# Kernel optimization log

Hardware: AMD Instinct MI355X
Metric: run time of the kernel (lower is better)

Reference implementation:

```python
import jax, jax.numpy as jnp
import numpy as np

N_QUBITS = 16
N_LAYERS = 8
BATCH = 512


def _apply_1q(st, U, wire):
    """Apply a 2x2 (or batched [B,2,2]) unitary on `wire` of st [B]+[2]*n."""
    st2 = jnp.moveaxis(st, wire + 1, -1)
    if U.ndim == 3:  # batched (input-encoding) gate
        out = jnp.einsum('sab,s...b->s...a', U, st2)
    else:
        out = jnp.einsum('ab,...b->...a', U, st2)
    return jnp.moveaxis(out, -1, wire + 1)


def _apply_cnot(st, c, t):
    """CNOT(control=c, target=t) on st [B]+[2]*n; axis of wire w is w+1."""
    s0, s1 = jnp.split(st, 2, axis=c + 1)
    s1 = jnp.flip(s1, axis=t + 1)  # X on target within control=1 block
    return jnp.concatenate([s0, s1], axis=c + 1)


def _rot_mats(w):
    """PennyLane Rot(phi,theta,omega)=RZ(omega)RY(theta)RZ(phi); w:[n,3] -> [n,2,2]."""
    phi, theta, omega = w[:, 0], w[:, 1], w[:, 2]
    c = jnp.cos(theta / 2).astype(jnp.complex64)
    s = jnp.sin(theta / 2).astype(jnp.complex64)
    ep = jnp.exp(-0.5j * (phi + omega))  # complex64
    em = jnp.exp(-0.5j * (phi - omega))
    m00 = ep * c
    m01 = -jnp.conj(em) * s
    m10 = em * s
    m11 = jnp.conj(ep) * c
    return jnp.stack([jnp.stack([m00, m01], -1), jnp.stack([m10, m11], -1)], -2)


def _circuit(x, weights):
    B, n = x.shape
    # |0...0> state, shape [B] + [2]*n
    st = jnp.zeros((B,) + (2,) * n, jnp.complex64)
    st = st.at[(slice(None),) + (0,) * n].set(1.0)
    # RY(pi * x_i) encoding on each wire (batched gates)
    a = (jnp.pi * x) / 2
    ca, sa = jnp.cos(a), jnp.sin(a)
    for i in range(n):
        U = jnp.stack([jnp.stack([ca[:, i], -sa[:, i]], -1),
                       jnp.stack([sa[:, i], ca[:, i]], -1)], -2).astype(jnp.complex64)
        st = _apply_1q(st, U, i)
    # StronglyEntanglingLayers: per-layer Rot on each wire, then ring of CNOTs
    for l in range(N_LAYERS):
        mats = _rot_mats(weights[l])
        for i in range(n):
            st = _apply_1q(st, mats[i], i)
        r = (l % (n - 1)) + 1  # default PennyLane range pattern
        for i in range(n):
            st = _apply_cnot(st, i, (i + r) % n)
    # <Z_i> = P(bit_i = 0) - P(bit_i = 1)
    p = st.real ** 2 + st.imag ** 2
    outs = []
    for i in range(n):
        marg = jnp.sum(p, axis=tuple(ax for ax in range(1, n + 1) if ax != i + 1))  # [B,2]
        outs.append(marg[:, 0] - marg[:, 1])
    return jnp.stack(outs, axis=-1).astype(jnp.float32)  # [B, n]


def setup_inputs() -> dict:
    key = jax.random.key(0)
    k1, k2 = jax.random.split(key)
    x = jax.random.uniform(k1, (BATCH, N_QUBITS), dtype=jnp.float32)
    weights = jax.random.uniform(k2, (N_LAYERS, N_QUBITS, 3), dtype=jnp.float32)
    return {"x": x, "weights": weights}


def reference(x, weights):
    return _circuit(x, weights)
```

## Files before the change

kernel.cpp:

```cpp
#include <hip/hip_runtime.h>
#include <cstring>

#define NQ 16
#define NLAYERS 8
#define BATCHN 512
#define GROUPB 128
#define NGROUP (BATCHN/GROUPB)
#define LB 13
#define NLOC (1<<LB)
#define NCHUNK (1<<(NQ-LB))
#define NTHREADS 512

typedef unsigned u32;

struct PD {
  int layerA, layerB, mode, b0;
  int qop[13];
  int glb[3];
  int r1dPos[2];
  int r1dQ[2];
  int r1lQ;
  int r1f[9];
  u32 tinv[13];
  u32 cinv[13];
  u32 tL[13];
  u32 cL[13];
  u32 tCkL[3];
  u32 fCk[3];
  u32 r1em[9];
  u32 r1eL[9];
  u32 r1dm[2];
  u32 r1dLm[2];
};

template<int J>
__device__ __forceinline__ void gate16(float2 (&a)[16],
  float M0r,float M0i,float M1r,float M1i,float M2r,float M2i,float M3r,float M3i){
  #pragma unroll
  for (int i=0;i<16;i++){
    if ((i>>J)&1) continue;
    const int i1 = i|(1<<J);
    float ar=a[i].x, ai=a[i].y, br=a[i1].x, bi=a[i1].y;
    a[i].x  = M0r*ar - M0i*ai + M1r*br - M1i*bi;
    a[i].y  = M0r*ai + M0i*ar + M1r*bi + M1i*br;
    a[i1].x = M2r*ar - M2i*ai + M3r*br - M3i*bi;
    a[i1].y = M2r*ai + M2i*ar + M3r*bi + M3i*br;
  }
}

__device__ __forceinline__ void lane_gate16(float2 (&a)[16], int tid, int j,
  float r0,float i0,float r1,float i1,float r2,float i2,float r3,float i3){
  int bit = (tid >> j) & 1;
  float cAr = bit? r3 : r0, cAi = bit? i3 : i0;
  float cBr = bit? r2 : r1, cBi = bit? i2 : i1;
  #pragma unroll
  for (int i=0;i<16;i++){
    float tx = __shfl_xor(a[i].x, 1<<j);
    float ty = __shfl_xor(a[i].y, 1<<j);
    float ax = a[i].x, ay = a[i].y;
    a[i].x = cAr*ax - cAi*ay + cBr*tx - cBi*ty;
    a[i].y = cAr*ay + cAi*ax + cBr*ty + cBi*tx;
  }
}

#define APPLY16(J, SRC) { \
  int _s = (SRC); \
  float r0_=__shfl(mm0,_s), i0_=__shfl(mm1,_s), r1_=__shfl(mm2,_s), i1_=__shfl(mm3,_s); \
  float r2_=__shfl(mm4,_s), i2_=__shfl(mm5,_s), r3_=__shfl(mm6,_s), i3_=__shfl(mm7,_s); \
  gate16<J>(a, r0_,i0_,r1_,i1_,r2_,i2_,r3_,i3_); }

#define LANE16(J, SRC) { \
  int _s = (SRC); \
  float r0_=__shfl(mm0,_s), i0_=__shfl(mm1,_s), r1_=__shfl(mm2,_s), i1_=__shfl(mm3,_s); \
  float r2_=__shfl(mm4,_s), i2_=__shfl(mm5,_s), r3_=__shfl(mm6,_s), i3_=__shfl(mm7,_s); \
  lane_gate16(a, tid, (J), r0_,i0_,r1_,i1_,r2_,i2_,r3_,i3_); }

__global__ __launch_bounds__(NTHREADS, 2)
void qpass(const float* __restrict__ x, const float* __restrict__ w,
           float2* __restrict__ state, float* __restrict__ out, PD pd)
{
  __shared__ __align__(16) float2 st[NLOC];
  const int tid = threadIdx.x;
  const u32 chunk = blockIdx.x;
  const int b = pd.b0 + blockIdx.y;
  float2* __restrict__ gst = state + ((size_t)b << NQ);

  float mm0,mm1,mm2,mm3,mm4,mm5,mm6,mm7;
  {
    int lane = tid & 63;
    int q = lane & 15;
    int lay = ((lane>>4)&1) ? pd.layerB : pd.layerA;
    if (lay < 0) lay = 0;
    float phi = w[(lay*NQ+q)*3+0], th = w[(lay*NQ+q)*3+1], om = w[(lay*NQ+q)*3+2];
    float sh, ch; sincosf(0.5f*th, &sh, &ch);
    float spo, cpo; sincosf(-0.5f*(phi+om), &spo, &cpo);
    float smo, cmo; sincosf(-0.5f*(phi-om), &smo, &cmo);
    mm0 =  cpo*ch; mm1 =  spo*ch;
    mm2 = -cmo*sh; mm3 =  smo*sh;
    mm4 =  cmo*sh; mm5 =  smo*sh;
    mm6 =  cpo*ch; mm7 = -spo*ch;
  }

  u32 ckL = 0;
  if (chunk & 1) ckL ^= pd.tCkL[0];
  if (chunk & 2) ckL ^= pd.tCkL[1];
  if (chunk & 4) ckL ^= pd.tCkL[2];

  float2 a[16];

  if (pd.mode != 1){
    u32 ebase = 0, lbL = 0;
    #pragma unroll
    for (int j=0;j<9;j++) if ((tid>>j)&1){ ebase ^= pd.r1em[j]; lbL ^= pd.r1eL[j]; }
    #pragma unroll
    for (int j=0;j<3;j++) if ((chunk>>j)&1) ebase ^= 1u<<pd.glb[j];
    #pragma unroll
    for (int g=0; g<4; g++){
      u32 full = ebase ^ ((g&1)?pd.r1dm[0]:0u) ^ (((g>>1)&1)?pd.r1dm[1]:0u);
      const float4* gp = (const float4*)(gst + full);
      float4 v0 = gp[0], v1 = gp[1];
      a[g*4+0] = make_float2(v0.x,v0.y); a[g*4+1] = make_float2(v0.z,v0.w);
      a[g*4+2] = make_float2(v1.x,v1.y); a[g*4+3] = make_float2(v1.z,v1.w);
    }
    APPLY16(2, pd.r1dQ[0]);
    APPLY16(3, pd.r1dQ[1]);
    LANE16(5, pd.r1lQ);

    if (pd.mode == 2){
      float acc[NQ];
      #pragma unroll
      for (int q=0;q<NQ;q++) acc[q]=0.f;
      u32 nb = 0;
      #pragma unroll
      for (int j=0;j<9;j++) if ((tid>>j)&1) nb ^= pd.cinv[pd.r1f[j]];
      #pragma unroll
      for (int j=0;j<3;j++) if ((chunk>>j)&1) nb ^= pd.fCk[j];
      u32 cd0 = pd.cinv[pd.r1dPos[0]], cd1 = pd.cinv[pd.r1dPos[1]];
      #pragma unroll
      for (int g=0; g<4; g++){
        u32 n0 = nb ^ ((g&1)?cd0:0u) ^ (((g>>1)&1)?cd1:0u);
        #pragma unroll
        for (int e=0;e<4;e++){
          u32 n = n0 ^ ((e&1)?pd.cinv[0]:0u) ^ (((e>>1)&1)?pd.cinv[1]:0u);
          float2 v = a[g*4+e];
          float p = v.x*v.x + v.y*v.y;
          #pragma unroll
          for (int q=0;q<NQ;q++) acc[q] += ((n>>q)&1u) ? -p : p;
        }
      }
      #pragma unroll
      for (int q=0;q<NQ;q++){
        float v = acc[q];
        #pragma unroll
        for (int off=32; off; off>>=1) v += __shfl_xor(v, off);
        if ((tid & 63) == 0) atomicAdd(&out[b*NQ+q], v);
      }
      return;
    }

    #pragma unroll
    for (int g=0; g<4; g++){
      u32 mL = lbL ^ ((g&1)?pd.r1dLm[0]:0u) ^ (((g>>1)&1)?pd.r1dLm[1]:0u);
      ((float4*)st)[(mL>>1)  ] = make_float4(a[g*4+0].x,a[g*4+0].y,a[g*4+1].x,a[g*4+1].y);
      ((float4*)st)[(mL>>1)+1] = make_float4(a[g*4+2].x,a[g*4+2].y,a[g*4+3].x,a[g*4+3].y);
    }
    __syncthreads();
  }

  u32 sbL = ckL;
  #pragma unroll
  for (int j=0;j<9;j++) if ((tid>>j)&1) sbL ^= pd.tL[2+j];
  const u32 Ltd0 = pd.tL[11], Ltd1 = pd.tL[12], Le0 = pd.tL[0], Le1 = pd.tL[1];

  if (pd.mode == 1){
    float ca[NQ], sa[NQ];
    #pragma unroll
    for (int q=0;q<NQ;q++){
      float aa = 1.57079632679489662f * x[b*NQ+q];
      sincosf(aa, &sa[q], &ca[q]);
    }
    float vt = 1.f;
    #pragma unroll
    for (int j=0;j<9;j++){ int q = pd.qop[2+j]; vt *= ((tid>>j)&1)? sa[q] : ca[q]; }
    #pragma unroll
    for (int j=0;j<3;j++){ int q = pd.glb[j]; vt *= ((chunk>>j)&1)? sa[q] : ca[q]; }
    float c0 = ca[pd.qop[0]], s0 = sa[pd.qop[0]], c1 = ca[pd.qop[1]], s1 = sa[pd.qop[1]];
    float cd0 = ca[pd.qop[11]], sd0 = sa[pd.qop[11]];
    float cd1 = ca[pd.qop[12]], sd1 = sa[pd.qop[12]];
    #pragma unroll
    for (int g=0; g<4; g++){
      float vg = vt * ((g&1)? sd0 : cd0) * (((g>>1)&1)? sd1 : cd1);
      a[g*4+0] = make_float2(vg*c0*c1, 0.f);
      a[g*4+1] = make_float2(vg*s0*c1, 0.f);
      a[g*4+2] = make_float2(vg*c0*s1, 0.f);
      a[g*4+3] = make_float2(vg*s0*s1, 0.f);
    }
  } else {
    #pragma unroll
    for (int g=0; g<4; g++){
      u32 sL = sbL ^ ((g&1)?Ltd0:0u) ^ (((g>>1)&1)?Ltd1:0u);
      a[g*4+0] = st[sL];
      a[g*4+1] = st[sL^Le0];
      a[g*4+2] = st[sL^Le1];
      a[g*4+3] = st[sL^Le0^Le1];
    }
  }

  APPLY16(0, 16+pd.qop[0]);  APPLY16(1, 16+pd.qop[1]);
  APPLY16(2, 16+pd.qop[11]); APPLY16(3, 16+pd.qop[12]);
  #pragma unroll
  for (int j=0;j<6;j++){
    LANE16(j, 16+pd.qop[2+j]);
  }

  #pragma unroll
  for (int g=0; g<4; g++){
    u32 sL = sbL ^ ((g&1)?Ltd0:0u) ^ (((g>>1)&1)?Ltd1:0u);
    st[sL]         = a[g*4+0];
    st[sL^Le0]     = a[g*4+1];
    st[sL^Le1]     = a[g*4+2];
    st[sL^Le0^Le1] = a[g*4+3];
  }
  __syncthreads();

  {
    u32 s2L = ckL;
    if (tid & 1) s2L ^= pd.tL[10];
    #pragma unroll
    for (int j=1;j<7;j++) if ((tid>>j)&1) s2L ^= pd.tL[1+j];
    if ((tid>>7)&1) s2L ^= pd.tL[11];
    if ((tid>>8)&1) s2L ^= pd.tL[12];
    const u32 LD0 = pd.tL[8], LD1 = pd.tL[9];
    #pragma unroll
    for (int g=0; g<4; g++){
      u32 sL = s2L ^ ((g&1)?LD0:0u) ^ (((g>>1)&1)?LD1:0u);
      a[g*4+0] = st[sL];
      a[g*4+1] = st[sL^Le0];
      a[g*4+2] = st[sL^Le1];
      a[g*4+3] = st[sL^Le0^Le1];
    }
    APPLY16(2, 16+pd.qop[8]); APPLY16(3, 16+pd.qop[9]);
    LANE16(0, 16+pd.qop[10]);
    #pragma unroll
    for (int g=0; g<4; g++){
      u32 sL = s2L ^ ((g&1)?LD0:0u) ^ (((g>>1)&1)?LD1:0u);
      st[sL]         = a[g*4+0];
      st[sL^Le0]     = a[g*4+1];
      st[sL^Le1]     = a[g*4+2];
      st[sL^Le0^Le1] = a[g*4+3];
    }
    __syncthreads();
  }

  {
    u32 ctL = ckL, etid = 0;
    #pragma unroll
    for (int j=0;j<9;j++) if ((tid>>j)&1){ ctL ^= pd.cL[2+j]; etid ^= 1u<<pd.qop[2+j]; }
    #pragma unroll
    for (int j=0;j<3;j++) if ((chunk>>j)&1) etid ^= 1u<<pd.glb[j];
    const u32 Lc0 = pd.cL[0], Lc1 = pd.cL[1];
    const u32 Lc11 = pd.cL[11], Lc12 = pd.cL[12];
    const u32 q11 = 1u<<pd.qop[11], q12 = 1u<<pd.qop[12];
    #pragma unroll
    for (int j=0;j<4;j++){
      u32 srcL  = ctL  ^ ((j&1)?Lc11:0u) ^ (((j>>1)&1)?Lc12:0u);
      u32 ofull = etid ^ ((j&1)?q11:0u)  ^ (((j>>1)&1)?q12:0u);
      float2 vv0 = st[srcL];
      float2 vv1 = st[srcL^Lc0];
      float2 vv2 = st[srcL^Lc1];
      float2 vv3 = st[srcL^Lc0^Lc1];
      float4* gp = (float4*)(gst + ofull);
      gp[0] = make_float4(vv0.x,vv0.y,vv1.x,vv1.y);
      gp[1] = make_float4(vv2.x,vv2.y,vv3.x,vv3.y);
    }
  }
}

static const int Gs[9][3] = {
  {13,14,15},{8,10,12},{11,13,15},{8,9,10},{7,11,15},{8,9,10},{11,12,13},{8,9,10},{13,14,15}
};
static const int Dlen[8] = {4,5,7,9,8,10,8,6};
static const int Dl[8][10] = {
  {12,13,14,15,0,0,0,0,0,0},
  {6,8,10,12,14,0,0,0,0,0},
  {8,10,11,12,13,14,15,0,0,0},
  {4,5,6,8,9,10,12,13,14,0},
  {2,6,7,10,11,12,13,15,0,0},
  {2,3,4,8,9,10,12,13,14,15},
  {4,5,6,11,12,13,14,15,0,0},
  {0,1,2,8,9,10,0,0,0,0},
};

static inline u32 apply_cnot_idx(u32 v, int c, int t){ return v ^ (((v>>c)&1u)<<t); }
static inline u32 h_swz(u32 q){ return q ^ ((q>>3)&7u); }
static inline u32 h_Lmap(u32 m){ return (h_swz(m>>2)<<2) | (m&3u); }

extern "C" void kernel_launch(void* const* d_in, const int* in_sizes, int n_in,
                              void* d_out, int out_size, void* d_ws, size_t ws_size,
                              hipStream_t stream)
{
  (void)in_sizes; (void)n_in; (void)ws_size;
  const float* x = (const float*)d_in[0];
  const float* w = (const float*)d_in[1];
  float* out = (float*)d_out;
  float2* state = (float2*)d_ws;

  hipMemsetAsync(d_out, 0, (size_t)out_size*sizeof(float), stream);

  for (int grp=0; grp<NGROUP; grp++){
    for (int p=0; p<9; p++){
      PD pd; memset(&pd, 0, sizeof(pd));
      pd.layerA = p-1;
      pd.layerB = (p<=7)? p : -1;
      pd.mode = (p==0)? 1 : ((p==8)? 2 : 0);
      pd.b0 = grp*GROUPB;

      u32 gm = 0;
      for (int i=0;i<3;i++){ pd.glb[i] = Gs[p][i]; gm |= 1u<<Gs[p][i]; }
      int np=0;
      for (int q=0;q<16;q++) if (!((gm>>q)&1u)) pd.qop[np++] = q;

      if (p >= 1){
        int pos[3], qq[3];
        for (int i=0;i<3;i++){
          int q = Gs[p-1][i]; qq[i] = q;
          int c=0; for (int k=0;k<q;k++) if ((gm>>k)&1u) c++;
          pos[i] = q - c;
        }
        for (int i=0;i<3;i++) for (int k=i+1;k<3;k++)
          if (pos[k] < pos[i]){ int t=pos[i];pos[i]=pos[k];pos[k]=t; t=qq[i];qq[i]=qq[k];qq[k]=t; }
        pd.r1lQ = qq[0];
        pd.r1dPos[0]=pos[1]; pd.r1dQ[0]=qq[1];
        pd.r1dPos[1]=pos[2]; pd.r1dQ[1]=qq[2];
        int free_[9], nf=0;
        for (int pp=2; pp<13; pp++)
          if (pp!=pos[0] && pp!=pos[1] && pp!=pos[2]) free_[nf++]=pp;
        for (int j=0;j<5;j++) pd.r1f[j]=free_[j];
        pd.r1f[5]=pos[0];
        for (int j=0;j<3;j++) pd.r1f[6+j]=free_[5+j];
      } else {
        pd.r1lQ = 0;
        pd.r1dPos[0]=11; pd.r1dQ[0]=0;
        pd.r1dPos[1]=12; pd.r1dQ[1]=0;
        for (int j=0;j<5;j++) pd.r1f[j]=2+j;
        pd.r1f[5]=10; pd.r1f[6]=7; pd.r1f[7]=8; pd.r1f[8]=9;
      }

      if (p == 0){
        for (int bp=0;bp<13;bp++) pd.tinv[bp] = 1u<<bp;
        for (int j=0;j<3;j++) pd.tCkL[j] = 0u;
      } else {
        int r = p;
        for (int bp=0;bp<13;bp++){
          u32 v = 1u<<pd.qop[bp];
          for (int i=Dlen[p-1]-1;i>=0;i--){ int c=Dl[p-1][i]; v = apply_cnot_idx(v, c, (c+r)&15); }
          u32 lv=0; for (int rr=0;rr<13;rr++) lv |= ((v>>pd.qop[rr])&1u)<<rr;
          pd.tinv[bp] = lv;
        }
        for (int j=0;j<3;j++){
          u32 v = 1u<<pd.glb[j];
          for (int i=Dlen[p-1]-1;i>=0;i--){ int c=Dl[p-1][i]; v = apply_cnot_idx(v, c, (c+r)&15); }
          v &= ~(1u<<pd.glb[j]);
          u32 lv=0; for (int rr=0;rr<13;rr++) lv |= ((v>>pd.qop[rr])&1u)<<rr;
          pd.tCkL[j] = h_Lmap(lv);
        }
      }

      if (p <= 7){
        int r = p+1;
        bool inD[16]; for (int i=0;i<16;i++) inD[i]=false;
        for (int i=0;i<Dlen[p];i++) inD[Dl[p][i]] = true;
        int A[16], na=0;
        for (int i=0;i<16;i++) if (!inD[i]) A[na++]=i;
        for (int bp=0;bp<13;bp++){
          u32 v = 1u<<pd.qop[bp];
          for (int i=na-1;i>=0;i--){ int c=A[i]; v = apply_cnot_idx(v, c, (c+r)&15); }
          if (p >= 1){
            int rp = p;
            for (int i=Dlen[p-1]-1;i>=0;i--){ int c=Dl[p-1][i]; v = apply_cnot_idx(v, c, (c+rp)&15); }
          }
          u32 lv=0; for (int rr=0;rr<13;rr++) lv |= ((v>>pd.qop[rr])&1u)<<rr;
          pd.cinv[bp] = lv;
        }
        for (int j=0;j<3;j++) pd.fCk[j] = 0u;
      } else {
        for (int bp=0;bp<13;bp++){
          u32 v = 1u<<pd.qop[bp];
          for (int i=0;i<Dlen[7];i++){ int c=Dl[7][i]; v = apply_cnot_idx(v, c, (c+8)&15); }
          pd.cinv[bp] = v;
        }
        for (int j=0;j<3;j++){
          u32 v = 1u<<pd.glb[j];
          for (int i=0;i<Dlen[7];i++){ int c=Dl[7][i]; v = apply_cnot_idx(v, c, (c+8)&15); }
          pd.fCk[j] = v;
        }
      }

      for (int k=0;k<13;k++){
        pd.tL[k] = h_Lmap(pd.tinv[k]);
        pd.cL[k] = (p<=7) ? h_Lmap(pd.cinv[k]) : 0u;
      }
      for (int j=0;j<9;j++){
        pd.r1em[j] = 1u<<pd.qop[pd.r1f[j]];
        pd.r1eL[j] = h_Lmap(1u<<pd.r1f[j]);
      }
      for (int j=0;j<2;j++){
        pd.r1dm[j]  = 1u<<pd.qop[pd.r1dPos[j]];
        pd.r1dLm[j] = h_Lmap(1u<<pd.r1dPos[j]);
      }

      hipLaunchKernelGGL(qpass, dim3(NCHUNK, GROUPB), dim3(NTHREADS), 0, stream,
                         x, w, state, out, pd);
    }
  }
}
```

Before: 3.293 ms.

## Double threads per block, halve per-thread amplitudes, and specialise kernels per mode

Each block now runs 1024 threads, and each thread holds 8 amplitudes instead of 16. The gate mapping is reworked to match: one more qubit moves from in-register gates to cross-lane shuffle gates, and the index tables and host precomputation are updated. The mode branch becomes a template parameter with three separate kernels. In the init kernel, per-qubit sin/cos arrays are replaced by a host-computed code table. The aim is lower register pressure and more waves to hide latency, at the cost of more shuffle traffic and bigger blocks that need larger barriers.

```diff
diff --git a/kernel.cpp b/kernel.cpp
--- a/kernel.cpp
+++ b/kernel.cpp
@@ -9,35 +9,35 @@
 #define LB 13
 #define NLOC (1<<LB)
 #define NCHUNK (1<<(NQ-LB))
-#define NTHREADS 512
+#define NTHREADS 1024
 
 typedef unsigned u32;
 
 struct PD {
-  int layerA, layerB, mode, b0;
+  int layerA, layerB, b0;
   int qop[13];
   int glb[3];
-  int r1dPos[2];
-  int r1dQ[2];
-  int r1lQ;
-  int r1f[9];
+  int r1dPos;
+  int r1dQ;
+  int r1l0Q, r1l1Q;
+  int r1f[10];
+  int code[16];
   u32 tinv[13];
   u32 cinv[13];
   u32 tL[13];
   u32 cL[13];
   u32 tCkL[3];
   u32 fCk[3];
-  u32 r1em[9];
-  u32 r1eL[9];
-  u32 r1dm[2];
-  u32 r1dLm[2];
+  u32 r1em[10];
+  u32 r1eL[10];
+  u32 r1dm, r1dLm;
 };
 
 template<int J>
-__device__ __forceinline__ void gate16(float2 (&a)[16],
+__device__ __forceinline__ void gate8(float2 (&a)[8],
   float M0r,float M0i,float M1r,float M1i,float M2r,float M2i,float M3r,float M3i){
   #pragma unroll
-  for (int i=0;i<16;i++){
+  for (int i=0;i<8;i++){
     if ((i>>J)&1) continue;
     const int i1 = i|(1<<J);
     float ar=a[i].x, ai=a[i].y, br=a[i1].x, bi=a[i1].y;
@@ -48,13 +48,13 @@
   }
 }
 
-__device__ __forceinline__ void lane_gate16(float2 (&a)[16], int tid, int j,
+__device__ __forceinline__ void lane_gate8(float2 (&a)[8], int tid, int j,
   float r0,float i0,float r1,float i1,float r2,float i2,float r3,float i3){
   int bit = (tid >> j) & 1;
   float cAr = bit? r3 : r0, cAi = bit? i3 : i0;
   float cBr = bit? r2 : r1, cBi = bit? i2 : i1;
   #pragma unroll
-  for (int i=0;i<16;i++){
+  for (int i=0;i<8;i++){
     float tx = __shfl_xor(a[i].x, 1<<j);
     float ty = __shfl_xor(a[i].y, 1<<j);
     float ax = a[i].x, ay = a[i].y;
@@ -63,21 +63,22 @@
   }
 }
 
-#define APPLY16(J, SRC) { \
+#define APPLY8(J, SRC) { \
   int _s = (SRC); \
   float r0_=__shfl(mm0,_s), i0_=__shfl(mm1,_s), r1_=__shfl(mm2,_s), i1_=__shfl(mm3,_s); \
   float r2_=__shfl(mm4,_s), i2_=__shfl(mm5,_s), r3_=__shfl(mm6,_s), i3_=__shfl(mm7,_s); \
-  gate16<J>(a, r0_,i0_,r1_,i1_,r2_,i2_,r3_,i3_); }
-
-#define LANE16(J, SRC) { \
+  gate8<J>(a, r0_,i0_,r1_,i1_,r2_,i2_,r3_,i3_); }
+
+#define LANE8(J, SRC) { \
   int _s = (SRC); \
   float r0_=__shfl(mm0,_s), i0_=__shfl(mm1,_s), r1_=__shfl(mm2,_s), i1_=__shfl(mm3,_s); \
   float r2_=__shfl(mm4,_s), i2_=__shfl(mm5,_s), r3_=__shfl(mm6,_s), i3_=__shfl(mm7,_s); \
-  lane_gate16(a, tid, (J), r0_,i0_,r1_,i1_,r2_,i2_,r3_,i3_); }
-
-__global__ __launch_bounds__(NTHREADS, 2)
-void qpass(const float* __restrict__ x, const float* __restrict__ w,
-           float2* __restrict__ state, float* __restrict__ out, PD pd)
+  lane_gate8(a, tid, (J), r0_,i0_,r1_,i1_,r2_,i2_,r3_,i3_); }
+
+template<int MODE>
+__device__ __forceinline__ void qbody(const float* __restrict__ x, const float* __restrict__ w,
+                                      float2* __restrict__ state, float* __restrict__ out,
+                                      const PD& pd)
 {
   __shared__ __align__(16) float2 st[NLOC];
   const int tid = threadIdx.x;
@@ -106,39 +107,39 @@
   if (chunk & 2) ckL ^= pd.tCkL[1];
   if (chunk & 4) ckL ^= pd.tCkL[2];
 
-  float2 a[16];
-
-  if (pd.mode != 1){
+  float2 a[8];
+
+  if (MODE != 1){
     u32 ebase = 0, lbL = 0;
     #pragma unroll
-    for (int j=0;j<9;j++) if ((tid>>j)&1){ ebase ^= pd.r1em[j]; lbL ^= pd.r1eL[j]; }
+    for (int j=0;j<10;j++) if ((tid>>j)&1){ ebase ^= pd.r1em[j]; lbL ^= pd.r1eL[j]; }
     #pragma unroll
     for (int j=0;j<3;j++) if ((chunk>>j)&1) ebase ^= 1u<<pd.glb[j];
     #pragma unroll
-    for (int g=0; g<4; g++){
-      u32 full = ebase ^ ((g&1)?pd.r1dm[0]:0u) ^ (((g>>1)&1)?pd.r1dm[1]:0u);
+    for (int g=0; g<2; g++){
+      u32 full = ebase ^ (g ? pd.r1dm : 0u);
       const float4* gp = (const float4*)(gst + full);
       float4 v0 = gp[0], v1 = gp[1];
       a[g*4+0] = make_float2(v0.x,v0.y); a[g*4+1] = make_float2(v0.z,v0.w);
       a[g*4+2] = make_float2(v1.x,v1.y); a[g*4+3] = make_float2(v1.z,v1.w);
     }
-    APPLY16(2, pd.r1dQ[0]);
-    APPLY16(3, pd.r1dQ[1]);
-    LANE16(5, pd.r1lQ);
-
-    if (pd.mode == 2){
+    APPLY8(2, pd.r1dQ);
+    LANE8(4, pd.r1l0Q);
+    LANE8(5, pd.r1l1Q);
+
+    if (MODE == 2){
       float acc[NQ];
       #pragma unroll
       for (int q=0;q<NQ;q++) acc[q]=0.f;
       u32 nb = 0;
       #pragma unroll
-      for (int j=0;j<9;j++) if ((tid>>j)&1) nb ^= pd.cinv[pd.r1f[j]];
+      for (int j=0;j<10;j++) if ((tid>>j)&1) nb ^= pd.cinv[pd.r1f[j]];
       #pragma unroll
       for (int j=0;j<3;j++) if ((chunk>>j)&1) nb ^= pd.fCk[j];
-      u32 cd0 = pd.cinv[pd.r1dPos[0]], cd1 = pd.cinv[pd.r1dPos[1]];
+      const u32 cd = pd.cinv[pd.r1dPos];
       #pragma unroll
-      for (int g=0; g<4; g++){
-        u32 n0 = nb ^ ((g&1)?cd0:0u) ^ (((g>>1)&1)?cd1:0u);
+      for (int g=0; g<2; g++){
+        u32 n0 = nb ^ (g ? cd : 0u);
         #pragma unroll
         for (int e=0;e<4;e++){
           u32 n = n0 ^ ((e&1)?pd.cinv[0]:0u) ^ (((e>>1)&1)?pd.cinv[1]:0u);
@@ -159,8 +160,8 @@
     }
 
     #pragma unroll
-    for (int g=0; g<4; g++){
-      u32 mL = lbL ^ ((g&1)?pd.r1dLm[0]:0u) ^ (((g>>1)&1)?pd.r1dLm[1]:0u);
+    for (int g=0; g<2; g++){
+      u32 mL = lbL ^ (g ? pd.r1dLm : 0u);
       ((float4*)st)[(mL>>1)  ] = make_float4(a[g*4+0].x,a[g*4+0].y,a[g*4+1].x,a[g*4+1].y);
       ((float4*)st)[(mL>>1)+1] = make_float4(a[g*4+2].x,a[g*4+2].y,a[g*4+3].x,a[g*4+3].y);
     }
@@ -169,27 +170,25 @@
 
   u32 sbL = ckL;
   #pragma unroll
-  for (int j=0;j<9;j++) if ((tid>>j)&1) sbL ^= pd.tL[2+j];
-  const u32 Ltd0 = pd.tL[11], Ltd1 = pd.tL[12], Le0 = pd.tL[0], Le1 = pd.tL[1];
-
-  if (pd.mode == 1){
-    float ca[NQ], sa[NQ];
+  for (int j=0;j<10;j++) if ((tid>>j)&1) sbL ^= pd.tL[2+j];
+  const u32 Ltd = pd.tL[12], Le0 = pd.tL[0], Le1 = pd.tL[1];
+
+  if (MODE == 1){
+    float vt = 1.f, c0=1.f,s0=0.f, c1=1.f,s1=0.f, cdd=1.f,sdd=0.f;
     #pragma unroll
     for (int q=0;q<NQ;q++){
       float aa = 1.57079632679489662f * x[b*NQ+q];
-      sincosf(aa, &sa[q], &ca[q]);
-    }
-    float vt = 1.f;
-    #pragma unroll
-    for (int j=0;j<9;j++){ int q = pd.qop[2+j]; vt *= ((tid>>j)&1)? sa[q] : ca[q]; }
-    #pragma unroll
-    for (int j=0;j<3;j++){ int q = pd.glb[j]; vt *= ((chunk>>j)&1)? sa[q] : ca[q]; }
-    float c0 = ca[pd.qop[0]], s0 = sa[pd.qop[0]], c1 = ca[pd.qop[1]], s1 = sa[pd.qop[1]];
-    float cd0 = ca[pd.qop[11]], sd0 = sa[pd.qop[11]];
-    float cd1 = ca[pd.qop[12]], sd1 = sa[pd.qop[12]];
-    #pragma unroll
-    for (int g=0; g<4; g++){
-      float vg = vt * ((g&1)? sd0 : cd0) * (((g>>1)&1)? sd1 : cd1);
+      float sq, cq; sincosf(aa, &sq, &cq);
+      int code = pd.code[q];
+      if (code < 10)        vt *= ((tid>>code)&1) ? sq : cq;
+      else if (code < 32)   vt *= ((chunk>>(code-16))&1) ? sq : cq;
+      else if (code == 32){ c0=cq; s0=sq; }
+      else if (code == 33){ c1=cq; s1=sq; }
+      else                { cdd=cq; sdd=sq; }
+    }
+    #pragma unroll
+    for (int g=0; g<2; g++){
+      float vg = vt * (g ? sdd : cdd);
       a[g*4+0] = make_float2(vg*c0*c1, 0.f);
       a[g*4+1] = make_float2(vg*s0*c1, 0.f);
       a[g*4+2] = make_float2(vg*c0*s1, 0.f);
@@ -197,8 +196,8 @@
     }
   } else {
     #pragma unroll
-    for (int g=0; g<4; g++){
-      u32 sL = sbL ^ ((g&1)?Ltd0:0u) ^ (((g>>1)&1)?Ltd1:0u);
+    for (int g=0; g<2; g++){
+      u32 sL = sbL ^ (g ? Ltd : 0u);
       a[g*4+0] = st[sL];
       a[g*4+1] = st[sL^Le0];
       a[g*4+2] = st[sL^Le1];
@@ -206,16 +205,15 @@
     }
   }
 
-  APPLY16(0, 16+pd.qop[0]);  APPLY16(1, 16+pd.qop[1]);
-  APPLY16(2, 16+pd.qop[11]); APPLY16(3, 16+pd.qop[12]);
+  APPLY8(0, 16+pd.qop[0]);  APPLY8(1, 16+pd.qop[1]);  APPLY8(2, 16+pd.qop[12]);
   #pragma unroll
   for (int j=0;j<6;j++){
-    LANE16(j, 16+pd.qop[2+j]);
+    LANE8(j, 16+pd.qop[2+j]);
   }
 
   #pragma unroll
-  for (int g=0; g<4; g++){
-    u32 sL = sbL ^ ((g&1)?Ltd0:0u) ^ (((g>>1)&1)?Ltd1:0u);
+  for (int g=0; g<2; g++){
+    u32 sL = sbL ^ (g ? Ltd : 0u);
     st[sL]         = a[g*4+0];
     st[sL^Le0]     = a[g*4+1];
     st[sL^Le1]     = a[g*4+2];
@@ -225,25 +223,28 @@
 
   {
     u32 s2L = ckL;
-    if (tid & 1) s2L ^= pd.tL[10];
-    #pragma unroll
-    for (int j=1;j<7;j++) if ((tid>>j)&1) s2L ^= pd.tL[1+j];
-    if ((tid>>7)&1) s2L ^= pd.tL[11];
-    if ((tid>>8)&1) s2L ^= pd.tL[12];
-    const u32 LD0 = pd.tL[8], LD1 = pd.tL[9];
-    #pragma unroll
-    for (int g=0; g<4; g++){
-      u32 sL = s2L ^ ((g&1)?LD0:0u) ^ (((g>>1)&1)?LD1:0u);
+    if (tid & 1)      s2L ^= pd.tL[8];
+    if ((tid>>1)&1)   s2L ^= pd.tL[9];
+    if ((tid>>2)&1)   s2L ^= pd.tL[10];
+    #pragma unroll
+    for (int j=3;j<9;j++) if ((tid>>j)&1) s2L ^= pd.tL[2+(j-3)];
+    if ((tid>>9)&1)   s2L ^= pd.tL[12];
+    const u32 LD = pd.tL[11];
+    #pragma unroll
+    for (int g=0; g<2; g++){
+      u32 sL = s2L ^ (g ? LD : 0u);
       a[g*4+0] = st[sL];
       a[g*4+1] = st[sL^Le0];
       a[g*4+2] = st[sL^Le1];
       a[g*4+3] = st[sL^Le0^Le1];
     }
-    APPLY16(2, 16+pd.qop[8]); APPLY16(3, 16+pd.qop[9]);
-    LANE16(0, 16+pd.qop[10]);
-    #pragma unroll
-    for (int g=0; g<4; g++){
-      u32 sL = s2L ^ ((g&1)?LD0:0u) ^ (((g>>1)&1)?LD1:0u);
+    APPLY8(2, 16+pd.qop[11]);
+    LANE8(0, 16+pd.qop[8]);
+    LANE8(1, 16+pd.qop[9]);
+    LANE8(2, 16+pd.qop[10]);
+    #pragma unroll
+    for (int g=0; g<2; g++){
+      u32 sL = s2L ^ (g ? LD : 0u);
       st[sL]         = a[g*4+0];
       st[sL^Le0]     = a[g*4+1];
       st[sL^Le1]     = a[g*4+2];
@@ -255,16 +256,16 @@
   {
     u32 ctL = ckL, etid = 0;
     #pragma unroll
-    for (int j=0;j<9;j++) if ((tid>>j)&1){ ctL ^= pd.cL[2+j]; etid ^= 1u<<pd.qop[2+j]; }
+    for (int j=0;j<10;j++) if ((tid>>j)&1){ ctL ^= pd.cL[2+j]; etid ^= 1u<<pd.qop[2+j]; }
     #pragma unroll
     for (int j=0;j<3;j++) if ((chunk>>j)&1) etid ^= 1u<<pd.glb[j];
     const u32 Lc0 = pd.cL[0], Lc1 = pd.cL[1];
-    const u32 Lc11 = pd.cL[11], Lc12 = pd.cL[12];
-    const u32 q11 = 1u<<pd.qop[11], q12 = 1u<<pd.qop[12];
-    #pragma unroll
-    for (int j=0;j<4;j++){
-      u32 srcL  = ctL  ^ ((j&1)?Lc11:0u) ^ (((j>>1)&1)?Lc12:0u);
-      u32 ofull = etid ^ ((j&1)?q11:0u)  ^ (((j>>1)&1)?q12:0u);
+    const u32 c12 = pd.cL[12];
+    const u32 q12m = 1u<<pd.qop[12];
+    #pragma unroll
+    for (int g=0; g<2; g++){
+      u32 srcL  = ctL  ^ (g ? c12  : 0u);
+      u32 ofull = etid ^ (g ? q12m : 0u);
       float2 vv0 = st[srcL];
       float2 vv1 = st[srcL^Lc0];
       float2 vv2 = st[srcL^Lc1];
@@ -275,6 +276,21 @@
     }
   }
 }
+
+__global__ __launch_bounds__(NTHREADS) __attribute__((amdgpu_waves_per_eu(4,8)))
+void qpass_mid(const float* __restrict__ x, const float* __restrict__ w,
+               float2* __restrict__ state, float* __restrict__ out, PD pd)
+{ qbody<0>(x,w,state,out,pd); }
+
+__global__ __launch_bounds__(NTHREADS) __attribute__((amdgpu_waves_per_eu(4,8)))
+void qpass_init(const float* __restrict__ x, const float* __restrict__ w,
+                float2* __restrict__ state, float* __restrict__ out, PD pd)
+{ qbody<1>(x,w,state,out,pd); }
+
+__global__ __launch_bounds__(NTHREADS) __attribute__((amdgpu_waves_per_eu(4,8)))
+void qpass_fin(const float* __restrict__ x, const float* __restrict__ w,
+               float2* __restrict__ state, float* __restrict__ out, PD pd)
+{ qbody<2>(x,w,state,out,pd); }
 
 static const int Gs[9][3] = {
   {13,14,15},{8,10,12},{11,13,15},{8,9,10},{7,11,15},{8,9,10},{11,12,13},{8,9,10},{13,14,15}
@@ -312,7 +328,6 @@
       PD pd; memset(&pd, 0, sizeof(pd));
       pd.layerA = p-1;
       pd.layerB = (p<=7)? p : -1;
-      pd.mode = (p==0)? 1 : ((p==8)? 2 : 0);
       pd.b0 = grp*GROUPB;
 
       u32 gm = 0;
@@ -329,21 +344,34 @@
         }
         for (int i=0;i<3;i++) for (int k=i+1;k<3;k++)
           if (pos[k] < pos[i]){ int t=pos[i];pos[i]=pos[k];pos[k]=t; t=qq[i];qq[i]=qq[k];qq[k]=t; }
-        pd.r1lQ = qq[0];
-        pd.r1dPos[0]=pos[1]; pd.r1dQ[0]=qq[1];
-        pd.r1dPos[1]=pos[2]; pd.r1dQ[1]=qq[2];
-        int free_[9], nf=0;
+        pd.r1l0Q = qq[0]; pd.r1l1Q = qq[1];
+        pd.r1dPos = pos[2]; pd.r1dQ = qq[2];
+        int free_[11], nf=0;
         for (int pp=2; pp<13; pp++)
           if (pp!=pos[0] && pp!=pos[1] && pp!=pos[2]) free_[nf++]=pp;
-        for (int j=0;j<5;j++) pd.r1f[j]=free_[j];
-        pd.r1f[5]=pos[0];
-        for (int j=0;j<3;j++) pd.r1f[6+j]=free_[5+j];
+        pd.r1f[0]=free_[0]; pd.r1f[1]=free_[1]; pd.r1f[2]=free_[2]; pd.r1f[3]=free_[3];
+        pd.r1f[4]=pos[0];  pd.r1f[5]=pos[1];
+        for (int j=0;j<4;j++) pd.r1f[6+j]=free_[4+j];
       } else {
-        pd.r1lQ = 0;
-        pd.r1dPos[0]=11; pd.r1dQ[0]=0;
-        pd.r1dPos[1]=12; pd.r1dQ[1]=0;
-        for (int j=0;j<5;j++) pd.r1f[j]=2+j;
-        pd.r1f[5]=10; pd.r1f[6]=7; pd.r1f[7]=8; pd.r1f[8]=9;
+        pd.r1l0Q = 0; pd.r1l1Q = 0;
+        pd.r1dPos = 12; pd.r1dQ = 0;
+        for (int j=0;j<10;j++) pd.r1f[j]=2+j;
+      }
+
+      {
+        int posOf[16]; for (int i=0;i<16;i++) posOf[i] = -1;
+        for (int pp=0;pp<13;pp++) posOf[pd.qop[pp]] = pp;
+        for (int q=0;q<16;q++){
+          int pp = posOf[q];
+          if (pp < 0){
+            int cb=0; for (int j=0;j<3;j++) if (pd.glb[j]==q) cb=j;
+            pd.code[q] = 16+cb;
+          }
+          else if (pp==0)  pd.code[q] = 32;
+          else if (pp==1)  pd.code[q] = 33;
+          else if (pp==12) pd.code[q] = 34;
+          else             pd.code[q] = pp-2;
+        }
       }
 
       if (p == 0){
@@ -400,17 +428,22 @@
         pd.tL[k] = h_Lmap(pd.tinv[k]);
         pd.cL[k] = (p<=7) ? h_Lmap(pd.cinv[k]) : 0u;
       }
-      for (int j=0;j<9;j++){
+      for (int j=0;j<10;j++){
         pd.r1em[j] = 1u<<pd.qop[pd.r1f[j]];
         pd.r1eL[j] = h_Lmap(1u<<pd.r1f[j]);
       }
-      for (int j=0;j<2;j++){
-        pd.r1dm[j]  = 1u<<pd.qop[pd.r1dPos[j]];
-        pd.r1dLm[j] = h_Lmap(1u<<pd.r1dPos[j]);
-      }
-
-      hipLaunchKernelGGL(qpass, dim3(NCHUNK, GROUPB), dim3(NTHREADS), 0, stream,
-                         x, w, state, out, pd);
+      pd.r1dm  = 1u<<pd.qop[pd.r1dPos];
+      pd.r1dLm = h_Lmap(1u<<pd.r1dPos);
+
+      if (p == 0)
+        hipLaunchKernelGGL(qpass_init, dim3(NCHUNK, GROUPB), dim3(NTHREADS), 0, stream,
+                           x, w, state, out, pd);
+      else if (p == 8)
+        hipLaunchKernelGGL(qpass_fin, dim3(NCHUNK, GROUPB), dim3(NTHREADS), 0, stream,
+                           x, w, state, out, pd);
+      else
+        hipLaunchKernelGGL(qpass_mid, dim3(NCHUNK, GROUPB), dim3(NTHREADS), 0, stream,
+                           x, w, state, out, pd);
     }
   }
 }
```

After: 3.215 ms. -2.4%, faster.
